# Kernel tuning notes

Measured on AMD Instinct MI355X. Metric: run time of the kernel, lower is better.

Reference implementation:

```python
import jax, jax.numpy as jnp
import numpy as np

N = 50000      # nodes
E = 800000     # edges (before self-loops)
F_IN = 128     # num_features
HID = 32       # hidden channels per head (conv1)
HEADS = 4      # conv1 heads
C = 40         # classes (conv2 out channels)
OUT_HEADS = 1  # conv2 heads
NEG_SLOPE = 0.2


def setup_inputs() -> dict:
    key = jax.random.key(0)
    ks = jax.random.split(key, 10)
    x = jax.random.normal(ks[0], (N, F_IN), jnp.float32)
    edge_index = jax.random.randint(ks[1], (2, E), 0, N, jnp.int32)
    s1 = 1.0 / np.sqrt(F_IN).astype(np.float32)
    s1h = 1.0 / np.sqrt(HID).astype(np.float32)
    s2 = 1.0 / np.sqrt(HEADS * HID).astype(np.float32)
    s2c = 1.0 / np.sqrt(C).astype(np.float32)
    W1 = jax.random.normal(ks[2], (F_IN, HEADS * HID), jnp.float32) * s1
    att_src1 = jax.random.normal(ks[3], (HEADS, HID), jnp.float32) * s1h
    att_dst1 = jax.random.normal(ks[4], (HEADS, HID), jnp.float32) * s1h
    bias1 = jnp.zeros((HEADS * HID,), jnp.float32)
    W2 = jax.random.normal(ks[5], (HEADS * HID, OUT_HEADS * C), jnp.float32) * s2
    att_src2 = jax.random.normal(ks[6], (OUT_HEADS, C), jnp.float32) * s2c
    att_dst2 = jax.random.normal(ks[7], (OUT_HEADS, C), jnp.float32) * s2c
    bias2 = jnp.zeros((C,), jnp.float32)
    return {"x": x, "edge_index": edge_index,
            "W1": W1, "att_src1": att_src1, "att_dst1": att_dst1, "bias1": bias1,
            "W2": W2, "att_src2": att_src2, "att_dst2": att_dst2, "bias2": bias2}


def gat_layer(h_in, src, dst, W, a_src, a_dst, bias, heads, out_ch, concat):
    """PyG GATConv (v1) in inference mode (no dropout on attention)."""
    n = h_in.shape[0]
    h = (h_in @ W).reshape(n, heads, out_ch)              # [N,H,F]
    e_src = jnp.einsum('nhf,hf->nh', h, a_src)            # [N,H]
    e_dst = jnp.einsum('nhf,hf->nh', h, a_dst)            # [N,H]
    alpha = jax.nn.leaky_relu(e_src[src] + e_dst[dst], NEG_SLOPE)  # [E,H]
    # segment softmax over destination-node neighborhoods
    amax = jax.ops.segment_max(alpha, dst, num_segments=n)
    amax = jnp.where(jnp.isfinite(amax), amax, 0.0)
    ex = jnp.exp(alpha - amax[dst])
    denom = jax.ops.segment_sum(ex, dst, num_segments=n)
    coef = ex / (denom[dst] + 1e-16)                      # [E,H]
    # scatter-aggregate weighted source messages
    out = jax.ops.segment_sum(h[src] * coef[:, :, None], dst, num_segments=n)  # [N,H,F]
    out = out.reshape(n, heads * out_ch) if concat else out.mean(axis=1)
    return out + bias


def reference(x, edge_index, W1, att_src1, att_dst1, bias1, W2, att_src2, att_dst2, bias2):
    n = x.shape[0]
    loop = jnp.arange(n, dtype=edge_index.dtype)          # GATConv adds self-loops
    src = jnp.concatenate([edge_index[0], loop])
    dst = jnp.concatenate([edge_index[1], loop])
    h = jax.nn.elu(gat_layer(x, src, dst, W1, att_src1, att_dst1, bias1, HEADS, HID, True))
    out = gat_layer(h, src, dst, W2, att_src2, att_dst2, bias2, OUT_HEADS, C, False)
    return (jax.nn.log_softmax(out, axis=1), jax.nn.softmax(out, axis=1))
```

## Files before the change

kernel.cpp:

```cpp
#include <hip/hip_runtime.h>
#include <hip/hip_bf16.h>

#define F1   128
#define H1   4
#define C2   40
#define NEG  0.2f
#define DS   96
#define EPB  6400
#define BCAP 5632

typedef __hip_bfloat16 bf16;
typedef float f32x2 __attribute__((ext_vector_type(2)));
typedef short s16x8 __attribute__((ext_vector_type(8)));
typedef float f32x4 __attribute__((ext_vector_type(4)));

__device__ __forceinline__ float ldf(const void* p, size_t i, int isbf) {
    return isbf ? __bfloat162float(((const bf16*)p)[i]) : ((const float*)p)[i];
}
__device__ __forceinline__ float lrelu(float a) { return a > 0.f ? a : NEG * a; }

__device__ __forceinline__ unsigned short f2bfb(float f, float& back) {
    unsigned u = __float_as_uint(f);
    unsigned r = u + 0x7FFFu + ((u >> 16) & 1u);
    unsigned short h = (unsigned short)(r >> 16);
    back = __uint_as_float((unsigned)h << 16);
    return h;
}

__device__ __forceinline__ void up2(unsigned g, float& lo, float& hi) {
    lo = __uint_as_float(g << 16);
    hi = __uint_as_float(g & 0xffff0000u);
}
__device__ __forceinline__ f32x2 up2v(unsigned g) {
    f32x2 r;
    r.x = __uint_as_float(g << 16);
    r.y = __uint_as_float(g & 0xffff0000u);
    return r;
}

__device__ __forceinline__ int excl_scan256(int v, int t, int* wsum) {
    int lane = t & 63, wid = t >> 6;
    int orig = v;
#pragma unroll
    for (int o = 1; o < 64; o <<= 1) {
        int n = __shfl_up(v, o, 64);
        if (lane >= o) v += n;
    }
    if (lane == 63) wsum[wid] = v;
    __syncthreads();
    int add = 0;
    for (int k = 0; k < wid; k++) add += wsum[k];
    return v + add - orig;
}

__global__ void k_prep(const unsigned short* __restrict__ x, int* __restrict__ gbin_cnt,
                       int* __restrict__ flag) {
    int t = threadIdx.x;
    gbin_cnt[t] = 0;
    __shared__ int sh[256];
    int cnt = 0;
    for (int k = t; k < 8192; k += 256)
        if (((x[k] >> 7) & 0xFF) >= 160) cnt++;
    sh[t] = cnt;
    __syncthreads();
    for (int s = 128; s > 0; s >>= 1) {
        if (t < s) sh[t] += sh[t + s];
        __syncthreads();
    }
    if (t == 0) flag[0] = (sh[0] < 100) ? 1 : 0;
}

__global__ void k_wprep(const void* __restrict__ W1, const int* __restrict__ flag,
                        unsigned short* __restrict__ w1t_hi,
                        unsigned short* __restrict__ w1t_lo) {
    int idx = blockIdx.x * 256 + threadIdx.x;
    int k = idx >> 7, c = idx & 127;
    const int isbf = flag[0];
    float v = ldf(W1, idx, isbf);
    float back;
    unsigned short hi = f2bfb(v, back);
    float d2;
    unsigned short lo = f2bfb(v - back, d2);
    w1t_hi[c * 128 + k] = hi;
    w1t_lo[c * 128 + k] = isbf ? (unsigned short)0 : lo;
}

__global__ void __launch_bounds__(256) k_scatA(
        const int* __restrict__ ei, int E, int ET, int nbins,
        int* __restrict__ gbin_cnt, unsigned long long* __restrict__ stg) {
    __shared__ int hist[256], lstart[256], gbase[256], lcnt[256];
    __shared__ int wsum[4];
    __shared__ unsigned long long stgl[EPB];
    int t = threadIdx.x;
    hist[t] = 0; lcnt[t] = 0;
    __syncthreads();
    int e0 = blockIdx.x * EPB;
    int e1 = e0 + EPB; if (e1 > ET) e1 = ET;
    for (int e = e0 + t; e < e1; e += 256) {
        int d = (e < E) ? ei[E + e] : (e - E);
        atomicAdd(&hist[d >> 8], 1);
    }
    __syncthreads();
    if (t < nbins && hist[t] > 0) gbase[t] = atomicAdd(&gbin_cnt[t], hist[t]);
    int ls = excl_scan256(hist[t], t, wsum);
    lstart[t] = ls;
    __syncthreads();
    for (int e = e0 + t; e < e1; e += 256) {
        int s, d;
        if (e < E) { s = ei[e]; d = ei[E + e]; }
        else       { s = e - E; d = e - E; }
        int b = d >> 8;
        int r = atomicAdd(&lcnt[b], 1);
        stgl[lstart[b] + r] = ((unsigned long long)(unsigned)d << 32) | (unsigned)s;
    }
    __syncthreads();
    int cntb = e1 - e0;
    for (int i = t; i < cntb; i += 256) {
        unsigned long long p = stgl[i];
        int d = (int)(p >> 32);
        int b = d >> 8;
        int off = gbase[b] + (i - lstart[b]);
        if (off < BCAP) stg[(size_t)b * BCAP + off] = p;
    }
}

__global__ void __launch_bounds__(256) k_scatB(
        const unsigned long long* __restrict__ stg, const int* __restrict__ gbin_cnt,
        int N, int* __restrict__ csr_s, int* __restrict__ rowstart,
        int* __restrict__ deg) {
    __shared__ int dhist[256], dstart[256], dcnt[256];
    __shared__ int wsum[4];
    __shared__ int out_s[BCAP];
    int bin = blockIdx.x, t = threadIdx.x;
    int cnt = gbin_cnt[bin]; if (cnt > BCAP) cnt = BCAP;
    dhist[t] = 0; dcnt[t] = 0;
    __syncthreads();
    const unsigned long long* mystg = stg + (size_t)bin * BCAP;
    for (int i = t; i < cnt; i += 256)
        atomicAdd(&dhist[(int)(mystg[i] >> 32) & 255], 1);
    __syncthreads();
    int ds = excl_scan256(dhist[t], t, wsum);
    dstart[t] = ds;
    __syncthreads();
    for (int i = t; i < cnt; i += 256) {
        unsigned long long p = mystg[i];
        int ld = (int)(p >> 32) & 255;
        int r = atomicAdd(&dcnt[ld], 1);
        out_s[dstart[ld] + r] = (int)(p & 0xffffffffu);
    }
    __syncthreads();
    size_t gb = (size_t)bin * BCAP;
    for (int i = t; i < cnt; i += 256) csr_s[gb + i] = out_s[i];
    int d = bin * 256 + t;
    if (d < N) { rowstart[d] = (int)gb + dstart[t]; deg[d] = dhist[t]; }
}

__global__ void __launch_bounds__(256) k_gemm1(
        const void* __restrict__ x, const unsigned short* __restrict__ w1t_hi,
        const unsigned short* __restrict__ w1t_lo,
        const void* __restrict__ as1, const void* __restrict__ ad1,
        const int* __restrict__ flag,
        bf16* __restrict__ h1b, float* __restrict__ es1, float* __restrict__ ed1,
        int N) {
    const int isbf = flag[0];
    int t = threadIdx.x, wv = t >> 6, l = t & 63;
    int r0 = (wv & 1) * 16, c0 = (wv >> 1) * 64;
    int lr = l & 15, q = l >> 4;
    int n0 = blockIdx.x * 32;
    int rowa = n0 + r0 + lr; if (rowa >= N) rowa = N - 1;

    const bf16*  xb = (const bf16*)x;
    const float* xf = (const float*)x;
    f32x4 acc[4] = {};

#pragma unroll
    for (int ks = 0; ks < 4; ks++) {
        int kb = ks * 32 + q * 8;
        s16x8 ahi, alo;
        if (isbf) {
            ahi = *(const s16x8*)&xb[(size_t)rowa * 128 + kb];
        } else {
            const float* xr = xf + (size_t)rowa * 128 + kb;
            float4 v0 = *(const float4*)xr;
            float4 v1 = *(const float4*)(xr + 4);
            float vv[8] = {v0.x, v0.y, v0.z, v0.w, v1.x, v1.y, v1.z, v1.w};
#pragma unroll
            for (int j = 0; j < 8; j++) {
                float back;
                unsigned short hb = f2bfb(vv[j], back);
                float d2;
                unsigned short lb = f2bfb(vv[j] - back, d2);
                ahi[j] = (short)hb;
                alo[j] = (short)lb;
            }
        }
#pragma unroll
        for (int f = 0; f < 4; f++) {
            int col = c0 + f * 16 + lr;
            s16x8 bh = *(const s16x8*)&w1t_hi[(size_t)col * 128 + kb];
            acc[f] = __builtin_amdgcn_mfma_f32_16x16x32_bf16(ahi, bh, acc[f], 0, 0, 0);
            if (!isbf) {
                s16x8 bl = *(const s16x8*)&w1t_lo[(size_t)col * 128 + kb];
                acc[f] = __builtin_amdgcn_mfma_f32_16x16x32_bf16(alo, bh, acc[f], 0, 0, 0);
                acc[f] = __builtin_amdgcn_mfma_f32_16x16x32_bf16(ahi, bl, acc[f], 0, 0, 0);
            }
        }
    }

    float asv[4], adv[4];
#pragma unroll
    for (int f = 0; f < 4; f++) {
        asv[f] = ldf(as1, c0 + f * 16 + lr, isbf);
        adv[f] = ldf(ad1, c0 + f * 16 + lr, isbf);
    }
    float ps0[4], ps1[4], pd0[4], pd1[4];
#pragma unroll
    for (int r = 0; r < 4; r++) {
        int rw = n0 + r0 + q * 4 + r;
        ps0[r] = acc[0][r] * asv[0] + acc[1][r] * asv[1];
        ps1[r] = acc[2][r] * asv[2] + acc[3][r] * asv[3];
        pd0[r] = acc[0][r] * adv[0] + acc[1][r] * adv[1];
        pd1[r] = acc[2][r] * adv[2] + acc[3][r] * adv[3];
        if (rw < N) {
#pragma unroll
            for (int f = 0; f < 4; f++)
                h1b[(size_t)rw * 128 + c0 + f * 16 + lr] = __float2bfloat16(acc[f][r]);
        }
    }
#pragma unroll
    for (int off = 1; off < 16; off <<= 1) {
#pragma unroll
        for (int r = 0; r < 4; r++) {
            ps0[r] += __shfl_xor(ps0[r], off, 64);
            ps1[r] += __shfl_xor(ps1[r], off, 64);
            pd0[r] += __shfl_xor(pd0[r], off, 64);
            pd1[r] += __shfl_xor(pd1[r], off, 64);
        }
    }
    if (lr == 0) {
        int h0 = c0 >> 5;
#pragma unroll
        for (int r = 0; r < 4; r++) {
            int rw = n0 + r0 + q * 4 + r;
            if (rw < N) {
                es1[rw * H1 + h0]     = ps0[r];
                es1[rw * H1 + h0 + 1] = ps1[r];
                ed1[rw * H1 + h0]     = pd0[r];
                ed1[rw * H1 + h0 + 1] = pd1[r];
            }
        }
    }
}

__global__ void __launch_bounds__(256) k_l1(
        const int* __restrict__ deg, const int* __restrict__ rowstart,
        const int* __restrict__ csr_s,
        const float* __restrict__ es1, const float* __restrict__ ed1,
        const uint4* __restrict__ h1p4, const void* __restrict__ b1,
        const void* __restrict__ W2, const void* __restrict__ as2,
        const void* __restrict__ ad2, const int* __restrict__ flag,
        bf16* __restrict__ h2b, float* __restrict__ es2, float* __restrict__ ed2,
        int N) {
    int w = threadIdx.x >> 6, l = threadIdx.x & 63;
    int d = blockIdx.x * 4 + w; if (d >= N) d = N - 1;
    int cnt = deg[d]; if (cnt > DS) cnt = DS;
    int start = rowstart[d];

    __shared__ int   s_sh[4][DS];
    __shared__ float ev_sh[4][4][DS + 4];
    __shared__ float hs[4][144];

    float4 edv = *(const float4*)&ed1[(size_t)d * 4];
    float t0 = 0.f, t1 = 0.f, t2 = 0.f, t3 = 0.f;
    if (l < cnt) {
        int s = csr_s[start + l];
        s_sh[w][l] = s;
        float4 es4 = *(const float4*)&es1[(size_t)s * 4];
        float v0 = __expf(lrelu(es4.x + edv.x));
        float v1 = __expf(lrelu(es4.y + edv.y));
        float v2 = __expf(lrelu(es4.z + edv.z));
        float v3 = __expf(lrelu(es4.w + edv.w));
        ev_sh[w][0][l] = v0; ev_sh[w][1][l] = v1;
        ev_sh[w][2][l] = v2; ev_sh[w][3][l] = v3;
        t0 = v0; t1 = v1; t2 = v2; t3 = v3;
    }
    if (cnt > 64) {
        int l2 = 64 + l;
        if (l2 < cnt) {
            int s = csr_s[start + l2];
            s_sh[w][l2] = s;
            float4 es4 = *(const float4*)&es1[(size_t)s * 4];
            float v0 = __expf(lrelu(es4.x + edv.x));
            float v1 = __expf(lrelu(es4.y + edv.y));
            float v2 = __expf(lrelu(es4.z + edv.z));
            float v3 = __expf(lrelu(es4.w + edv.w));
            ev_sh[w][0][l2] = v0; ev_sh[w][1][l2] = v1;
            ev_sh[w][2][l2] = v2; ev_sh[w][3][l2] = v3;
            t0 += v0; t1 += v1; t2 += v2; t3 += v3;
        }
    }
#pragma unroll
    for (int o = 32; o > 0; o >>= 1) {
        t0 += __shfl_xor(t0, o, 64);
        t1 += __shfl_xor(t1, o, 64);
        t2 += __shfl_xor(t2, o, 64);
        t3 += __shfl_xor(t3, o, 64);
    }
    __syncthreads();

    int q = l >> 4, c16 = l & 15, h = c16 >> 2;
    f32x2 acc[4] = {{0.f, 0.f}, {0.f, 0.f}, {0.f, 0.f}, {0.f, 0.f}};
    for (int i = 0; i < cnt; i += 16) {
#pragma unroll
        for (int u = 0; u < 4; u++) {
            int e = i + q + 4 * u;
            int ec = min(e, cnt - 1);
            float evh = (e < cnt) ? ev_sh[w][h][ec] : 0.f;
            int s = s_sh[w][ec];
            uint4 g = h1p4[(size_t)s * 16 + c16];
            f32x2 ev2 = {evh, evh};
            acc[0] += ev2 * up2v(g.x);
            acc[1] += ev2 * up2v(g.y);
            acc[2] += ev2 * up2v(g.z);
            acc[3] += ev2 * up2v(g.w);
        }
    }

#pragma unroll
    for (int o = 16; o <= 32; o <<= 1) {
#pragma unroll
        for (int jj = 0; jj < 4; jj++) {
            acc[jj].x += __shfl_xor(acc[jj].x, o, 64);
            acc[jj].y += __shfl_xor(acc[jj].y, o, 64);
        }
    }

    const int isbf = flag[0];
    float dsum = (h == 0) ? t0 : (h == 1) ? t1 : (h == 2) ? t2 : t3;
    if (q == 0) {
        float inv = 1.f / (dsum + 1e-16f);
#pragma unroll
        for (int j = 0; j < 8; j++) {
            int col = c16 * 8 + j;
            float av = (j & 1) ? acc[j >> 1].y : acc[j >> 1].x;
            float v = av * inv + ldf(b1, col, isbf);
            hs[w][col + (col >> 3)] = v > 0.f ? v : (__expf(v) - 1.f);
        }
    }
    __syncthreads();
    float a2 = 0.f;
    if (l < C2) {
        if (isbf) {
            const bf16* W = (const bf16*)W2;
#pragma unroll 8
            for (int k = 0; k < F1; k++)
                a2 = fmaf(hs[w][k + (k >> 3)], __bfloat162float(W[(size_t)k * C2 + l]), a2);
        } else {
            const float* W = (const float*)W2;
#pragma unroll 8
            for (int k = 0; k < F1; k++)
                a2 = fmaf(hs[w][k + (k >> 3)], W[(size_t)k * C2 + l], a2);
        }
        h2b[(size_t)d * C2 + l] = __float2bfloat16(a2);
    }
    float ps = (l < C2) ? a2 * ldf(as2, l, isbf) : 0.f;
    float pd = (l < C2) ? a2 * ldf(ad2, l, isbf) : 0.f;
#pragma unroll
    for (int o = 32; o > 0; o >>= 1) {
        ps += __shfl_xor(ps, o, 64);
        pd += __shfl_xor(pd, o, 64);
    }
    if (l == 0) { es2[d] = ps; ed2[d] = pd; }
}

__global__ void __launch_bounds__(256) k_l2(
        const int* __restrict__ deg, const int* __restrict__ rowstart,
        const int* __restrict__ csr_s,
        const float* __restrict__ es2, const float* __restrict__ ed2,
        const unsigned* __restrict__ h2p, const void* __restrict__ b2,
        const int* __restrict__ flag, void* __restrict__ out, int N) {
    int w = threadIdx.x >> 6, l = threadIdx.x & 63;
    int d = blockIdx.x * 4 + w; if (d >= N) d = N - 1;
    int cnt = deg[d]; if (cnt > DS) cnt = DS;
    int start = rowstart[d];
    float edd = ed2[d];

    __shared__ int   s_sh2[4][DS];
    __shared__ float x_sh[4][DS];

    float xv = 0.f;
    if (l < cnt) {
        int s = csr_s[start + l];
        s_sh2[w][l] = s;
        xv = __expf(lrelu(es2[s] + edd));
        x_sh[w][l] = xv;
    }
    float dsum = xv;
    if (cnt > 64) {
        int l2 = 64 + l;
        if (l2 < cnt) {
            int s = csr_s[start + l2];
            s_sh2[w][l2] = s;
            float x2 = __expf(lrelu(es2[s] + edd));
            x_sh[w][l2] = x2;
            dsum += x2;
        }
    }
#pragma unroll
    for (int o = 32; o > 0; o >>= 1) dsum += __shfl_xor(dsum, o, 64);
    __syncthreads();

    int half = l >> 5, j = l & 31;
    float acc0 = 0.f, acc1 = 0.f;
    if (j < 20) {
        for (int i = 0; i < cnt; i += 16) {
#pragma unroll
            for (int u = 0; u < 8; u++) {
                int e = i + half * 8 + u;
                int ec = min(e, cnt - 1);
                float x = (e < cnt) ? x_sh[w][ec] : 0.f;
                int s = s_sh2[w][ec];
                unsigned g = h2p[(size_t)s * 20 + j];
                float lo, hi; up2(g, lo, hi);
                acc0 = fmaf(x, lo, acc0);
                acc1 = fmaf(x, hi, acc1);
            }
        }
        acc0 += __shfl_xor(acc0, 32, 64);
        acc1 += __shfl_xor(acc1, 32, 64);
    }

    const int isbf = flag[0];
    float inv = 1.f / (dsum + 1e-16f);
    float v0 = -1e30f, v1 = -1e30f;
    if (l < 20) {
        v0 = acc0 * inv + ldf(b2, 2 * l, isbf);
        v1 = acc1 * inv + ldf(b2, 2 * l + 1, isbf);
    }
    float m = fmaxf(v0, v1);
#pragma unroll
    for (int o = 16; o > 0; o >>= 1) m = fmaxf(m, __shfl_xor(m, o, 32));
    float sv = (l < 20) ? __expf(v0 - m) + __expf(v1 - m) : 0.f;
#pragma unroll
    for (int o = 16; o > 0; o >>= 1) sv += __shfl_xor(sv, o, 32);
    float lse = m + __logf(sv);
    if (l < 20) {
        float ls0 = v0 - lse, ls1 = v1 - lse;
        size_t base = (size_t)d * C2 + 2 * l, halfo = (size_t)N * C2;
        if (isbf) {
            bf16* o = (bf16*)out;
            o[base] = __float2bfloat16(ls0);
            o[base + 1] = __float2bfloat16(ls1);
            o[halfo + base] = __float2bfloat16(__expf(ls0));
            o[halfo + base + 1] = __float2bfloat16(__expf(ls1));
        } else {
            float* o = (float*)out;
            o[base] = ls0;
            o[base + 1] = ls1;
            o[halfo + base] = __expf(ls0);
            o[halfo + base + 1] = __expf(ls1);
        }
    }
}

extern "C" void kernel_launch(void* const* d_in, const int* in_sizes, int n_in,
                              void* d_out, int out_size, void* d_ws, size_t ws_size,
                              hipStream_t stream) {
    const int N  = in_sizes[0] / F1;
    const int E  = in_sizes[1] / 2;
    const int ET = E + N;
    const int NBINS = (N + 255) >> 8;

    const void* x   = d_in[0];
    const int*  ei  = (const int*)d_in[1];
    const void* W1  = d_in[2];
    const void* as1 = d_in[3];
    const void* ad1 = d_in[4];
    const void* b1  = d_in[5];
    const void* W2  = d_in[6];
    const void* as2 = d_in[7];
    const void* ad2 = d_in[8];
    const void* b2  = d_in[9];

    float* ws = (float*)d_ws;
    auto al4 = [](size_t v) { return (v + 3) & ~(size_t)3; };
    size_t o = 0;
    bf16*  h1b  = (bf16*)(ws + o); o = al4(o + (size_t)64 * N);
    float* es1  = ws + o; o = al4(o + (size_t)H1 * N);
    float* ed1  = ws + o; o = al4(o + (size_t)H1 * N);
    bf16*  h2b  = (bf16*)(ws + o); o = al4(o + (size_t)20 * N);
    float* es2  = ws + o; o = al4(o + N);
    float* ed2  = ws + o; o = al4(o + N);
    int*   deg  = (int*)(ws + o); o = al4(o + N);
    int*   rowstart = (int*)(ws + o); o = al4(o + N);
    int*   gbin_cnt = (int*)(ws + o); o = al4(o + 256);
    int*   flag = (int*)(ws + o); o = al4(o + 4);
    int*   csr_s = (int*)(ws + o); o = al4(o + (size_t)NBINS * BCAP);
    unsigned short* w1t_hi = (unsigned short*)(ws + o); o = al4(o + 8192);
    unsigned short* w1t_lo = (unsigned short*)(ws + o); o = al4(o + 8192);
    unsigned long long* stg = (unsigned long long*)(ws + o);
    o = al4(o + (size_t)2 * NBINS * BCAP);

    k_prep<<<1, 256, 0, stream>>>((const unsigned short*)x, gbin_cnt, flag);
    k_wprep<<<64, 256, 0, stream>>>(W1, flag, w1t_hi, w1t_lo);
    k_scatA<<<(ET + EPB - 1) / EPB, 256, 0, stream>>>(ei, E, ET, NBINS, gbin_cnt, stg);
    k_scatB<<<NBINS, 256, 0, stream>>>(stg, gbin_cnt, N, csr_s, rowstart, deg);
    k_gemm1<<<(N + 31) / 32, 256, 0, stream>>>(x, w1t_hi, w1t_lo, as1, ad1, flag,
                                               h1b, es1, ed1, N);
    k_l1<<<(N + 3) / 4, 256, 0, stream>>>(deg, rowstart, csr_s, es1, ed1,
                                          (const uint4*)h1b, b1, W2, as2, ad2, flag,
                                          h2b, es2, ed2, N);
    k_l2<<<(N + 3) / 4, 256, 0, stream>>>(deg, rowstart, csr_s, es2, ed2,
                                          (const unsigned*)h2b, b2, flag, d_out, N);
}
```

Measured before the change: 289.8 us.

## Fuse prep kernels, merge CSR bin sort into GEMM1, widen layer-2 gathers

Merges the dtype-detection and W1 transpose kernels into one 64-block launch, with every block recomputing the flag itself. Folds the per-bin CSR sort (k_scatB) into the first NBINS blocks of k_gemm1, removing two launches. Rewrites the layer-2 aggregation so each lane gathers 4 channels with uint2 loads, covering 4 edges per wave step, and writes float4 outputs. The costs are redundant flag scans in every prep block and extra shared memory in k_gemm1, which may lower its occupancy. The GEMM blocks may also run concurrently with the sort blocks they do not depend on.

```diff
diff --git a/kernel.cpp b/kernel.cpp
--- a/kernel.cpp
+++ b/kernel.cpp
@@ -53,10 +53,11 @@
     return v + add - orig;
 }
 
-__global__ void k_prep(const unsigned short* __restrict__ x, int* __restrict__ gbin_cnt,
-                       int* __restrict__ flag) {
+__global__ void k_prep(const unsigned short* __restrict__ x, const void* __restrict__ W1,
+                       int* __restrict__ gbin_cnt, int* __restrict__ flag,
+                       unsigned short* __restrict__ w1t_hi,
+                       unsigned short* __restrict__ w1t_lo) {
     int t = threadIdx.x;
-    gbin_cnt[t] = 0;
     __shared__ int sh[256];
     int cnt = 0;
     for (int k = t; k < 8192; k += 256)
@@ -67,15 +68,13 @@
         if (t < s) sh[t] += sh[t + s];
         __syncthreads();
     }
-    if (t == 0) flag[0] = (sh[0] < 100) ? 1 : 0;
-}
-
-__global__ void k_wprep(const void* __restrict__ W1, const int* __restrict__ flag,
-                        unsigned short* __restrict__ w1t_hi,
-                        unsigned short* __restrict__ w1t_lo) {
-    int idx = blockIdx.x * 256 + threadIdx.x;
+    const int isbf = (sh[0] < 100) ? 1 : 0;
+    if (blockIdx.x == 0) {
+        gbin_cnt[t] = 0;
+        if (t == 0) flag[0] = isbf;
+    }
+    int idx = blockIdx.x * 256 + t;
     int k = idx >> 7, c = idx & 127;
-    const int isbf = flag[0];
     float v = ldf(W1, idx, isbf);
     float back;
     unsigned short hi = f2bfb(v, back);
@@ -124,44 +123,43 @@
     }
 }
 
-__global__ void __launch_bounds__(256) k_scatB(
-        const unsigned long long* __restrict__ stg, const int* __restrict__ gbin_cnt,
-        int N, int* __restrict__ csr_s, int* __restrict__ rowstart,
-        int* __restrict__ deg) {
-    __shared__ int dhist[256], dstart[256], dcnt[256];
-    __shared__ int wsum[4];
-    __shared__ int out_s[BCAP];
-    int bin = blockIdx.x, t = threadIdx.x;
-    int cnt = gbin_cnt[bin]; if (cnt > BCAP) cnt = BCAP;
-    dhist[t] = 0; dcnt[t] = 0;
-    __syncthreads();
-    const unsigned long long* mystg = stg + (size_t)bin * BCAP;
-    for (int i = t; i < cnt; i += 256)
-        atomicAdd(&dhist[(int)(mystg[i] >> 32) & 255], 1);
-    __syncthreads();
-    int ds = excl_scan256(dhist[t], t, wsum);
-    dstart[t] = ds;
-    __syncthreads();
-    for (int i = t; i < cnt; i += 256) {
-        unsigned long long p = mystg[i];
-        int ld = (int)(p >> 32) & 255;
-        int r = atomicAdd(&dcnt[ld], 1);
-        out_s[dstart[ld] + r] = (int)(p & 0xffffffffu);
-    }
-    __syncthreads();
-    size_t gb = (size_t)bin * BCAP;
-    for (int i = t; i < cnt; i += 256) csr_s[gb + i] = out_s[i];
-    int d = bin * 256 + t;
-    if (d < N) { rowstart[d] = (int)gb + dstart[t]; deg[d] = dhist[t]; }
-}
-
 __global__ void __launch_bounds__(256) k_gemm1(
         const void* __restrict__ x, const unsigned short* __restrict__ w1t_hi,
         const unsigned short* __restrict__ w1t_lo,
         const void* __restrict__ as1, const void* __restrict__ ad1,
         const int* __restrict__ flag,
+        const unsigned long long* __restrict__ stg, const int* __restrict__ gbin_cnt,
+        int nbins, int* __restrict__ csr_s, int* __restrict__ rowstart,
+        int* __restrict__ deg,
         bf16* __restrict__ h1b, float* __restrict__ es1, float* __restrict__ ed1,
         int N) {
+    if (blockIdx.x < nbins) {
+        __shared__ int dhist[256], dstart[256], dcnt[256];
+        __shared__ int wsum[4];
+        __shared__ int out_s[BCAP];
+        int bin = blockIdx.x, tt = threadIdx.x;
+        int bcnt = gbin_cnt[bin]; if (bcnt > BCAP) bcnt = BCAP;
+        dhist[tt] = 0; dcnt[tt] = 0;
+        __syncthreads();
+        const unsigned long long* mystg = stg + (size_t)bin * BCAP;
+        for (int i = tt; i < bcnt; i += 256)
+            atomicAdd(&dhist[(int)(mystg[i] >> 32) & 255], 1);
+        __syncthreads();
+        int dsx = excl_scan256(dhist[tt], tt, wsum);
+        dstart[tt] = dsx;
+        __syncthreads();
+        for (int i = tt; i < bcnt; i += 256) {
+            unsigned long long p = mystg[i];
+            int ld = (int)(p >> 32) & 255;
+            int r = atomicAdd(&dcnt[ld], 1);
+            out_s[dstart[ld] + r] = (int)(p & 0xffffffffu);
+        }
+        __syncthreads();
+        size_t gb = (size_t)bin * BCAP;
+        for (int i = tt; i < bcnt; i += 256) csr_s[gb + i] = out_s[i];
+        int dd = bin * 256 + tt;
+        if (dd < N) { rowstart[dd] = (int)gb + dstart[tt]; deg[dd] = dhist[tt]; }
+    }
     const int isbf = flag[0];
     int t = threadIdx.x, wv = t >> 6, l = t & 63;
     int r0 = (wv & 1) * 16, c0 = (wv >> 1) * 64;
@@ -377,7 +375,7 @@
         const int* __restrict__ deg, const int* __restrict__ rowstart,
         const int* __restrict__ csr_s,
         const float* __restrict__ es2, const float* __restrict__ ed2,
-        const unsigned* __restrict__ h2p, const void* __restrict__ b2,
+        const uint2* __restrict__ h2p2, const void* __restrict__ b2,
         const int* __restrict__ flag, void* __restrict__ out, int N) {
     int w = threadIdx.x >> 6, l = threadIdx.x & 63;
     int d = blockIdx.x * 4 + w; if (d >= N) d = N - 1;
@@ -410,55 +408,65 @@
     for (int o = 32; o > 0; o >>= 1) dsum += __shfl_xor(dsum, o, 64);
     __syncthreads();
 
-    int half = l >> 5, j = l & 31;
-    float acc0 = 0.f, acc1 = 0.f;
-    if (j < 20) {
-        for (int i = 0; i < cnt; i += 16) {
-#pragma unroll
-            for (int u = 0; u < 8; u++) {
-                int e = i + half * 8 + u;
-                int ec = min(e, cnt - 1);
-                float x = (e < cnt) ? x_sh[w][ec] : 0.f;
-                int s = s_sh2[w][ec];
-                unsigned g = h2p[(size_t)s * 20 + j];
-                float lo, hi; up2(g, lo, hi);
-                acc0 = fmaf(x, lo, acc0);
-                acc1 = fmaf(x, hi, acc1);
+    int q = l >> 4, c10 = l & 15;
+    bool act = c10 < 10;
+    f32x2 acc0 = {0.f, 0.f}, acc1 = {0.f, 0.f};
+    for (int i = 0; i < cnt; i += 16) {
+#pragma unroll
+        for (int u = 0; u < 4; u++) {
+            int e = i + q + 4 * u;
+            int ec = min(e, cnt - 1);
+            float xc = (e < cnt) ? x_sh[w][ec] : 0.f;
+            int s = s_sh2[w][ec];
+            if (act) {
+                uint2 g = h2p2[(size_t)s * 10 + c10];
+                f32x2 x2 = {xc, xc};
+                acc0 += x2 * up2v(g.x);
+                acc1 += x2 * up2v(g.y);
             }
         }
-        acc0 += __shfl_xor(acc0, 32, 64);
-        acc1 += __shfl_xor(acc1, 32, 64);
+    }
+#pragma unroll
+    for (int o = 16; o <= 32; o <<= 1) {
+        acc0.x += __shfl_xor(acc0.x, o, 64); acc0.y += __shfl_xor(acc0.y, o, 64);
+        acc1.x += __shfl_xor(acc1.x, o, 64); acc1.y += __shfl_xor(acc1.y, o, 64);
     }
 
     const int isbf = flag[0];
     float inv = 1.f / (dsum + 1e-16f);
-    float v0 = -1e30f, v1 = -1e30f;
-    if (l < 20) {
-        v0 = acc0 * inv + ldf(b2, 2 * l, isbf);
-        v1 = acc1 * inv + ldf(b2, 2 * l + 1, isbf);
-    }
-    float m = fmaxf(v0, v1);
-#pragma unroll
-    for (int o = 16; o > 0; o >>= 1) m = fmaxf(m, __shfl_xor(m, o, 32));
-    float sv = (l < 20) ? __expf(v0 - m) + __expf(v1 - m) : 0.f;
-#pragma unroll
-    for (int o = 16; o > 0; o >>= 1) sv += __shfl_xor(sv, o, 32);
+    float v0 = -1e30f, v1 = -1e30f, v2 = -1e30f, v3 = -1e30f;
+    if (act) {
+        v0 = acc0.x * inv + ldf(b2, 4 * c10 + 0, isbf);
+        v1 = acc0.y * inv + ldf(b2, 4 * c10 + 1, isbf);
+        v2 = acc1.x * inv + ldf(b2, 4 * c10 + 2, isbf);
+        v3 = acc1.y * inv + ldf(b2, 4 * c10 + 3, isbf);
+    }
+    float m = fmaxf(fmaxf(v0, v1), fmaxf(v2, v3));
+#pragma unroll
+    for (int o = 8; o > 0; o >>= 1) m = fmaxf(m, __shfl_xor(m, o, 16));
+    float sv = act ? __expf(v0 - m) + __expf(v1 - m) + __expf(v2 - m) + __expf(v3 - m)
+                   : 0.f;
+#pragma unroll
+    for (int o = 8; o > 0; o >>= 1) sv += __shfl_xor(sv, o, 16);
     float lse = m + __logf(sv);
-    if (l < 20) {
-        float ls0 = v0 - lse, ls1 = v1 - lse;
-        size_t base = (size_t)d * C2 + 2 * l, halfo = (size_t)N * C2;
+    if (act && q == 0) {
+        float ls0 = v0 - lse, ls1 = v1 - lse, ls2 = v2 - lse, ls3 = v3 - lse;
+        size_t base = (size_t)d * C2 + 4 * c10, halfo = (size_t)N * C2;
         if (isbf) {
-            bf16* o = (bf16*)out;
-            o[base] = __float2bfloat16(ls0);
-            o[base + 1] = __float2bfloat16(ls1);
-            o[halfo + base] = __float2bfloat16(__expf(ls0));
-            o[halfo + base + 1] = __float2bfloat16(__expf(ls1));
+            bf16* o2 = (bf16*)out;
+            o2[base + 0] = __float2bfloat16(ls0);
+            o2[base + 1] = __float2bfloat16(ls1);
+            o2[base + 2] = __float2bfloat16(ls2);
+            o2[base + 3] = __float2bfloat16(ls3);
+            o2[halfo + base + 0] = __float2bfloat16(__expf(ls0));
+            o2[halfo + base + 1] = __float2bfloat16(__expf(ls1));
+            o2[halfo + base + 2] = __float2bfloat16(__expf(ls2));
+            o2[halfo + base + 3] = __float2bfloat16(__expf(ls3));
         } else {
-            float* o = (float*)out;
-            o[base] = ls0;
-            o[base + 1] = ls1;
-            o[halfo + base] = __expf(ls0);
-            o[halfo + base + 1] = __expf(ls1);
+            float4 lsv = {ls0, ls1, ls2, ls3};
+            *(float4*)((float*)out + base) = lsv;
+            float4 pv = {__expf(ls0), __expf(ls1), __expf(ls2), __expf(ls3)};
+            *(float4*)((float*)out + halfo + base) = pv;
         }
     }
 }
@@ -501,15 +509,15 @@
     unsigned long long* stg = (unsigned long long*)(ws + o);
     o = al4(o + (size_t)2 * NBINS * BCAP);
 
-    k_prep<<<1, 256, 0, stream>>>((const unsigned short*)x, gbin_cnt, flag);
-    k_wprep<<<64, 256, 0, stream>>>(W1, flag, w1t_hi, w1t_lo);
+    k_prep<<<64, 256, 0, stream>>>((const unsigned short*)x, W1, gbin_cnt, flag,
+                                   w1t_hi, w1t_lo);
     k_scatA<<<(ET + EPB - 1) / EPB, 256, 0, stream>>>(ei, E, ET, NBINS, gbin_cnt, stg);
-    k_scatB<<<NBINS, 256, 0, stream>>>(stg, gbin_cnt, N, csr_s, rowstart, deg);
     k_gemm1<<<(N + 31) / 32, 256, 0, stream>>>(x, w1t_hi, w1t_lo, as1, ad1, flag,
-                                               h1b, es1, ed1, N);
+                                               stg, gbin_cnt, NBINS, csr_s, rowstart,
+                                               deg, h1b, es1, ed1, N);
     k_l1<<<(N + 3) / 4, 256, 0, stream>>>(deg, rowstart, csr_s, es1, ed1,
                                           (const uint4*)h1b, b1, W2, as2, ad2, flag,
                                           h2b, es2, ed2, N);
     k_l2<<<(N + 3) / 4, 256, 0, stream>>>(deg, rowstart, csr_s, es2, ed2,
-                                          (const unsigned*)h2b, b2, flag, d_out, N);
-}
+                                          (const uint2*)h2b, b2, flag, d_out, N);
+}
```

New measurement: 283.0 us. -2.4%, faster.
